# Kernel optimization log

Measured on AMD Instinct MI355X. Metric: run time of the kernel, lower is better.

Reference implementation:

```python
import jax, jax.numpy as jnp
import numpy as np

HIDDEN = 3072
HEADS = 24
HEAD_DIM = HIDDEN // HEADS  # 128
MLP_HIDDEN = 4 * HIDDEN     # 12288
IMG_LEN = 1024
TXT_LEN = 256
L = IMG_LEN + TXT_LEN
B = 1
EPS = 1e-6


def setup_inputs() -> dict:
    key = jax.random.key(0)
    ks = jax.random.split(key, 12)
    x = jax.random.normal(ks[0], (B, L, HIDDEN), jnp.float32)
    vec = jax.random.normal(ks[1], (B, HIDDEN), jnp.float32)
    # RoPE tables: real cos/sin of position * inv_freq, repeated over pairs (full head_dim)
    inv_freq = 1.0 / (10000.0 ** (np.arange(0, HEAD_DIM, 2, dtype=np.float32) / HEAD_DIM))
    theta = np.arange(IMG_LEN, dtype=np.float32)[:, None] * inv_freq[None, :]  # [img_len, D/2]
    theta = np.repeat(theta, 2, axis=-1)  # [img_len, D]
    freqs_cos = jnp.asarray(np.cos(theta))[None, :, None, :]  # [1, img_len, 1, D]
    freqs_sin = jnp.asarray(np.sin(theta))[None, :, None, :]
    s = 0.02
    mod_w = jax.random.normal(ks[2], (HIDDEN, 3 * HIDDEN), jnp.float32) * s
    mod_b = jnp.zeros((3 * HIDDEN,), jnp.float32)
    w1 = jax.random.normal(ks[3], (HIDDEN, 3 * HIDDEN + MLP_HIDDEN), jnp.float32) * s
    b1 = jnp.zeros((3 * HIDDEN + MLP_HIDDEN,), jnp.float32)
    w2 = jax.random.normal(ks[4], (HIDDEN + MLP_HIDDEN, HIDDEN), jnp.float32) * s
    b2 = jnp.zeros((HIDDEN,), jnp.float32)
    qn_w = jnp.ones((HEAD_DIM,), jnp.float32)
    kn_w = jnp.ones((HEAD_DIM,), jnp.float32)
    cu_seqlens_q = jnp.array([0, IMG_LEN, L], jnp.int32)
    cu_seqlens_kv = jnp.array([0, IMG_LEN, L], jnp.int32)
    return {"x": x, "vec": vec, "freqs_cos": freqs_cos, "freqs_sin": freqs_sin,
            "mod_w": mod_w, "mod_b": mod_b, "w1": w1, "b1": b1, "w2": w2, "b2": b2,
            "qn_w": qn_w, "kn_w": kn_w, "img_len": IMG_LEN,
            "cu_seqlens_q": cu_seqlens_q, "cu_seqlens_kv": cu_seqlens_kv}


def _layernorm(x):  # elementwise_affine=False
    mu = jnp.mean(x, axis=-1, keepdims=True)
    var = jnp.mean(jnp.square(x - mu), axis=-1, keepdims=True)
    return (x - mu) * jax.lax.rsqrt(var + EPS)


def _rmsnorm(x, w):
    ms = jnp.mean(jnp.square(x), axis=-1, keepdims=True)
    return x * jax.lax.rsqrt(ms + EPS) * w


def _rope_interleaved(x, cos, sin):
    # mode=1: rotate interleaved pairs: (-x1, x0, -x3, x2, ...)
    x0 = x[..., 0::2]
    x1 = x[..., 1::2]
    rot = jnp.stack([-x1, x0], axis=-1).reshape(x.shape)
    return x * cos + rot * sin


def reference(x, vec, freqs_cos, freqs_sin, mod_w, mod_b, w1, b1, w2, b2,
              qn_w, kn_w, img_len, cu_seqlens_q, cu_seqlens_kv):
    bs = x.shape[0]
    assert cu_seqlens_q.shape[0] == 2 * bs + 1
    # adaLN modulation: SiLU -> Linear(hidden, 3*hidden)
    mod = jax.nn.silu(vec) @ mod_w + mod_b           # [B, 3H]
    mod = mod[:, None, :]                             # [B, 1, 3H]
    mod_shift, mod_scale, mod_gate = jnp.split(mod, 3, axis=-1)
    x_mod = _layernorm(x) * (1.0 + mod_scale) + mod_shift
    # fused QKV + MLP projection
    h = x_mod @ w1 + b1                               # [B, L, 3*hidden + mlp]
    qkv = h[..., :3 * HIDDEN]
    mlp = h[..., 3 * HIDDEN:]
    # 'B L (K H D) -> K B L H D'
    qkv = qkv.reshape(bs, -1, 3, HEADS, HEAD_DIM)
    q, k, v = qkv[:, :, 0], qkv[:, :, 1], qkv[:, :, 2]  # [B, L, H, D]
    q = _rmsnorm(q, qn_w)
    k = _rmsnorm(k, kn_w)
    # RoPE on image tokens only
    img_q = _rope_interleaved(q[:, :img_len], freqs_cos, freqs_sin)
    img_k = _rope_interleaved(k[:, :img_len], freqs_cos, freqs_sin)
    q = jnp.concatenate([img_q, q[:, img_len:]], axis=1)
    k = jnp.concatenate([img_k, k[:, img_len:]], axis=1)
    # dense attention (bs==1 path, no mask), scale = 1/sqrt(head_dim)
    scale = 1.0 / jnp.sqrt(jnp.float32(HEAD_DIM))
    scores = jnp.einsum('bqhd,bkhd->bhqk', q, k) * scale
    probs = jax.nn.softmax(scores, axis=-1)
    attn = jnp.einsum('bhqk,bkhd->bqhd', probs, v)
    attn = attn.reshape(bs, -1, HEADS * HEAD_DIM)     # [B, L, hidden]
    # output projection on concat(attn, gelu_tanh(mlp))
    out = jnp.concatenate([attn, jax.nn.gelu(mlp, approximate=True)], axis=-1) @ w2 + b2
    return x + out * mod_gate
```

## Files before the change

### kernel.cpp

```cpp
#include <hip/hip_runtime.h>
#include <cstdint>
#include <cstddef>

typedef __bf16 bf16x8_t __attribute__((ext_vector_type(8)));
typedef float f32x4 __attribute__((ext_vector_type(4)));

#define HID 3072
#define NHEADS 24
#define HD 128
#define MLP 12288
#define SEQ 1280
#define IMG 1024
#define N1 21504
#define QKVW 9216
#define A2W 15360
#define EPSV 1e-6f

__device__ __forceinline__ size_t tpos(int row, int col, int KT) {
    return ((size_t)(row >> 8) * KT + (col >> 6)) * 16384
         + (size_t)(((((col >> 5) & 1) << 4) + ((row >> 4) & 15)) * 512
                    + (((row & 15) + (((col >> 3) & 3) << 4)) << 3) + (col & 7));
}

__device__ __forceinline__ void gload16(const void* g, void* l) {
    __builtin_amdgcn_global_load_lds(
        (const __attribute__((address_space(1))) unsigned int*)g,
        (__attribute__((address_space(3))) unsigned int*)l, 16, 0, 0);
}

__device__ __forceinline__ void bar() {
    asm volatile("" ::: "memory");
    __builtin_amdgcn_s_barrier();
    asm volatile("" ::: "memory");
}

__device__ __forceinline__ float bf2f(uint u) {
    return __builtin_bit_cast(float, u << 16);
}
__device__ __forceinline__ ushort f2bfu(float f) {
    return __builtin_bit_cast(ushort, (__bf16)f);
}

__device__ __forceinline__ void conv_tile(const float* __restrict__ in, ushort* __restrict__ out,
                                          int N, int KT, int kb, int nb, int tid,
                                          float (*tle)[65]) {
    int k0 = kb * 64, n0 = nb * 64;
    int rr = tid >> 2, cg = (tid & 3) * 16;
    #pragma unroll
    for (int j = 0; j < 4; ++j) {
        float4 vv = *reinterpret_cast<const float4*>(&in[(size_t)(k0 + rr) * N + n0 + cg + j * 4]);
        tle[rr][cg + j * 4 + 0] = vv.x;
        tle[rr][cg + j * 4 + 1] = vv.y;
        tle[rr][cg + j * 4 + 2] = vv.z;
        tle[rr][cg + j * 4 + 3] = vv.w;
    }
    __syncthreads();
    int nl = tid & 63;
    #pragma unroll
    for (int gg = 0; gg < 2; ++gg) {
        int g = (tid >> 6) + gg * 4;
        union { ushort u[8]; uint4 q; } pk;
        #pragma unroll
        for (int j = 0; j < 8; ++j)
            pk.u[j] = f2bfu(tle[g * 8 + j][nl]);
        *reinterpret_cast<uint4*>(&out[tpos(n0 + nl, k0 + g * 8, KT)]) = pk.q;
    }
}

__global__ void silu_kernel(const float* __restrict__ v, float* __restrict__ sv) {
    int i = blockIdx.x * 256 + threadIdx.x;
    float x = v[i];
    sv[i] = x / (1.f + expf(-x));
}

__global__ __launch_bounds__(256) void gemvconv_fat(const float* __restrict__ sv,
                                                    const float* __restrict__ W,
                                                    float* __restrict__ part,
                                                    const float* __restrict__ w1,
                                                    ushort* __restrict__ w1b) {
    __shared__ float tle[64][65];
    int bid = blockIdx.x;
    int tid = threadIdx.x;
    if (bid < 288) {
        int n = (bid % 36) * 256 + tid;
        int k0 = (bid / 36) * 384;
        float s = 0.f;
        for (int k = k0; k < k0 + 384; ++k)
            s = fmaf(sv[k], W[(size_t)k * QKVW + n], s);
        part[(size_t)(bid / 36) * QKVW + n] = s;
        return;
    }
    int cb = bid - 288;
    conv_tile(w1, w1b, N1, HID / 64, cb % 48, cb / 48, tid, tle);
}

__global__ void gemv_reduce(const float* __restrict__ part, const float* __restrict__ bias,
                            float* __restrict__ mod) {
    int n = blockIdx.x * 256 + threadIdx.x;
    float s = bias[n];
    #pragma unroll
    for (int ky = 0; ky < 8; ++ky) s += part[(size_t)ky * QKVW + n];
    mod[n] = s;
}

__global__ __launch_bounds__(384) void ln_mod_kernel(const float* __restrict__ x,
                                                     const float* __restrict__ mod,
                                                     ushort* __restrict__ xmt) {
    int m = blockIdx.x;
    int t = threadIdx.x;
    int lane = t & 63, w = t >> 6;
    const float* xr = x + (size_t)m * HID;
    float4 v0 = *reinterpret_cast<const float4*>(&xr[t * 8]);
    float4 v1 = *reinterpret_cast<const float4*>(&xr[t * 8 + 4]);
    float s = v0.x + v0.y + v0.z + v0.w + v1.x + v1.y + v1.z + v1.w;
    float sq = v0.x * v0.x + v0.y * v0.y + v0.z * v0.z + v0.w * v0.w +
               v1.x * v1.x + v1.y * v1.y + v1.z * v1.z + v1.w * v1.w;
    #pragma unroll
    for (int off = 1; off < 64; off <<= 1) {
        s += __shfl_xor(s, off);
        sq += __shfl_xor(sq, off);
    }
    __shared__ float red[12];
    if (lane == 0) { red[w] = s; red[w + 6] = sq; }
    __syncthreads();
    s = red[0] + red[1] + red[2] + red[3] + red[4] + red[5];
    sq = red[6] + red[7] + red[8] + red[9] + red[10] + red[11];
    float mu = s * (1.f / HID);
    float var = sq * (1.f / HID) - mu * mu;
    float rs = rsqrtf(var + EPSV);
    float vals[8] = {v0.x, v0.y, v0.z, v0.w, v1.x, v1.y, v1.z, v1.w};
    union { ushort u[8]; uint4 q; } pk;
    #pragma unroll
    for (int j = 0; j < 8; ++j) {
        int n = t * 8 + j;
        float y = (vals[j] - mu) * rs * (1.f + mod[HID + n]) + mod[n];
        pk.u[j] = f2bfu(y);
    }
    *reinterpret_cast<uint4*>(&xmt[tpos(m, t * 8, HID >> 6)]) = pk.q;
}

template <int EPI, int SPLITS>
__global__ __launch_bounds__(512, 2) void gemmk(
    const ushort* __restrict__ At, const ushort* __restrict__ Bt,
    const float* __restrict__ bias, ushort* __restrict__ out1, ushort* __restrict__ out2,
    int KT64, int NT32, int NTN) {
    int nwg = gridDim.x;
    int q = nwg >> 3, r = nwg & 7;
    int orig = blockIdx.x;
    int xcd = orig & 7;
    int wgid = (xcd < r ? xcd * (q + 1) : r * (q + 1) + (xcd - r) * q) + (orig >> 3);
    int mt = wgid % 5;
    int p = wgid / 5;
    int nt = p % NTN;
    int sp = p / NTN;
    int kOff = sp * NT32;
    int m0 = mt * 256, n0 = nt * 256;

    __shared__ ushort LA[4][8192];
    __shared__ ushort LB[4][8192];

    int tid = threadIdx.x;
    int lane = tid & 63, wid = tid >> 6;
    int wm = wid >> 2, wn = wid & 3;
    int lr = lane & 15, lg = lane >> 4;

    const ushort* gA = At + (size_t)mt * KT64 * 16384;
    const ushort* gB = Bt + (size_t)nt * KT64 * 16384;

    f32x4 acc[8][4] = {};
    bf16x8_t af[8], bf[4];

    auto stage = [&](int sl, int tt) {
        size_t base = (size_t)(tt >> 1) * 16384 + (size_t)(tt & 1) * 8192;
        #pragma unroll
        for (int j = 0; j < 2; ++j) {
            int b = wid * 2 + j;
            gload16(gA + base + b * 512 + lane * 8, &LA[sl][b * 512]);
            gload16(gB + base + b * 512 + lane * 8, &LB[sl][b * 512]);
        }
    };

    stage(0, kOff); stage(1, kOff + 1); stage(2, kOff + 2); stage(3, kOff + 3);
    asm volatile("s_waitcnt vmcnt(12)" ::: "memory");
    bar();

    for (int t = 0; t < NT32; ++t) {
        int sl = t & 3;
        #pragma unroll
        for (int mi = 0; mi < 8; ++mi)
            af[mi] = *reinterpret_cast<const bf16x8_t*>(&LA[sl][(wm * 8 + mi) * 512 + lane * 8]);
        #pragma unroll
        for (int nj = 0; nj < 4; ++nj)
            bf[nj] = *reinterpret_cast<const bf16x8_t*>(&LB[sl][(wn * 4 + nj) * 512 + lane * 8]);
        __builtin_amdgcn_s_setprio(1);
        #pragma unroll
        for (int mi = 0; mi < 8; ++mi)
            #pragma unroll
            for (int nj = 0; nj < 4; ++nj)
                acc[mi][nj] = __builtin_amdgcn_mfma_f32_16x16x32_bf16(af[mi], bf[nj], acc[mi][nj], 0, 0, 0);
        __builtin_amdgcn_s_setprio(0);
        bar();
        if (t + 4 < NT32) {
            stage(sl, kOff + t + 4);
            asm volatile("s_waitcnt vmcnt(12)" ::: "memory");
        } else if (t + 3 < NT32) {
            asm volatile("s_waitcnt vmcnt(8)" ::: "memory");
        } else if (t + 2 < NT32) {
            asm volatile("s_waitcnt vmcnt(4)" ::: "memory");
        } else if (t + 1 < NT32) {
            asm volatile("s_waitcnt vmcnt(0)" ::: "memory");
        }
        bar();
    }

    #pragma unroll
    for (int mi = 0; mi < 8; ++mi) {
        #pragma unroll
        for (int nj = 0; nj < 4; ++nj) {
            int col = n0 + wn * 64 + nj * 16 + lr;
            #pragma unroll
            for (int rr2 = 0; rr2 < 4; ++rr2) {
                int row = m0 + wm * 128 + mi * 16 + lg * 4 + rr2;
                float val = acc[mi][nj][rr2];
                if (EPI == 1) {
                    val += bias[col];
                    if (n0 < QKVW) {
                        out1[(size_t)row * QKVW + col] = f2bfu(val);
                    } else {
                        float u = 0.7978845608028654f * (val + 0.044715f * val * val * val);
                        float g = val / (1.f + __expf(-2.f * u));
                        out2[tpos(row, HID + (col - QKVW), A2W >> 6)] = f2bfu(g);
                    }
                } else {
                    out1[(size_t)(sp * SEQ + row) * HID + col] = f2bfu(val);
                }
            }
        }
    }
}

__global__ __launch_bounds__(256) void ksplit_reduce(const ushort* __restrict__ partb,
                                                     const float* __restrict__ x,
                                                     const float* __restrict__ bias,
                                                     const float* __restrict__ gate,
                                                     float* __restrict__ out) {
    size_t i = (size_t)blockIdx.x * 256 + threadIdx.x;
    int col = (int)((i * 8) % HID);
    float a[8] = {};
    #pragma unroll
    for (int s = 0; s < 4; ++s) {
        uint4 pv = *reinterpret_cast<const uint4*>(&partb[(size_t)s * SEQ * HID + i * 8]);
        uint w[4] = {pv.x, pv.y, pv.z, pv.w};
        #pragma unroll
        for (int c = 0; c < 4; ++c) {
            a[c * 2]     += bf2f(w[c] & 0xffffu);
            a[c * 2 + 1] += __builtin_bit_cast(float, w[c] & 0xffff0000u);
        }
    }
    f32x4 o0, o1;
    #pragma unroll
    for (int j = 0; j < 4; ++j) {
        o0[j] = x[i * 8 + j] + (a[j] + bias[col + j]) * gate[col + j];
        o1[j] = x[i * 8 + 4 + j] + (a[4 + j] + bias[col + 4 + j]) * gate[col + 4 + j];
    }
    *reinterpret_cast<f32x4*>(&out[i * 8]) = o0;
    *reinterpret_cast<f32x4*>(&out[i * 8 + 4]) = o1;
}

__global__ __launch_bounds__(256) void qkv_post(const ushort* __restrict__ hb,
                                                const float* __restrict__ fc,
                                                const float* __restrict__ fs,
                                                const float* __restrict__ qn,
                                                const float* __restrict__ kn,
                                                __bf16* __restrict__ qb,
                                                __bf16* __restrict__ kb,
                                                __bf16* __restrict__ vb) {
    int m = blockIdx.x;
    int lane = threadIdx.x & 63, w = threadIdx.x >> 6;
    for (int rr = w; rr < 72; rr += 4) {
        int s = rr / 24, hd = rr % 24;
        const ushort* src = hb + (size_t)m * QKVW + s * HID + hd * HD;
        uint pair = *reinterpret_cast<const uint*>(&src[2 * lane]);
        float x0 = bf2f(pair & 0xffffu);
        float x1 = __builtin_bit_cast(float, pair & 0xffff0000u);
        if (s < 2) {
            float ss = x0 * x0 + x1 * x1;
            #pragma unroll
            for (int off = 1; off < 64; off <<= 1) ss += __shfl_xor(ss, off);
            float rs = rsqrtf(ss * (1.f / HD) + EPSV);
            const float* nw = (s == 0) ? qn : kn;
            x0 *= rs * nw[2 * lane];
            x1 *= rs * nw[2 * lane + 1];
            if (m < IMG) {
                float c0 = fc[m * HD + 2 * lane], c1 = fc[m * HD + 2 * lane + 1];
                float s0 = fs[m * HD + 2 * lane], s1 = fs[m * HD + 2 * lane + 1];
                float r0 = x0 * c0 - x1 * s0;
                float r1 = x1 * c1 + x0 * s1;
                x0 = r0; x1 = r1;
            }
        }
        __bf16* dst = ((s == 0) ? qb : (s == 1) ? kb : vb) + (size_t)hd * SEQ * HD + (size_t)m * HD + 2 * lane;
        uint u0 = f2bfu(x0), u1 = f2bfu(x1);
        *reinterpret_cast<uint*>(dst) = u0 | (u1 << 16);
    }
}

__global__ __launch_bounds__(256) void attn_fat(const __bf16* __restrict__ qb,
                                                const __bf16* __restrict__ kb,
                                                const __bf16* __restrict__ vb,
                                                ushort* __restrict__ a2,
                                                const float* __restrict__ w2,
                                                ushort* __restrict__ w2b) {
    __shared__ float tle[64][65];
    int bid = blockIdx.x;
    int tid = threadIdx.x;
    if (bid >= 480) {
        int cb = bid - 480;
        conv_tile(w2, w2b, HID, A2W / 64, cb % 240, cb / 240, tid, tle);
        return;
    }
    __shared__ alignas(16) __bf16 Kl[32][136];
    __shared__ alignas(16) __bf16 Vl[32][136];
    __shared__ float Pl[4][32][16];

    int head = bid / 20;
    int lane = tid & 63, w = tid >> 6;
    int lr = lane & 15, lg = lane >> 4;
    int q0 = (bid % 20) * 64 + w * 16;
    const __bf16* Q = qb + (size_t)head * SEQ * HD;
    const __bf16* Kp = kb + (size_t)head * SEQ * HD;
    const __bf16* Vp = vb + (size_t)head * SEQ * HD;

    bf16x8_t qf[4];
    #pragma unroll
    for (int kc = 0; kc < 4; ++kc)
        qf[kc] = *reinterpret_cast<const bf16x8_t*>(&Q[(size_t)(q0 + lr) * HD + kc * 32 + lg * 8]);

    float m_run = -1e30f, l_run = 0.f;
    f32x4 of[8] = {};
    const float sm_scale = 0.08838834764831845f;

    for (int kv0 = 0; kv0 < SEQ; kv0 += 32) {
        #pragma unroll
        for (int cc = 0; cc < 2; ++cc) {
            int c = tid + cc * 256;
            int row = c >> 4, off = (c & 15) * 8;
            *reinterpret_cast<bf16x8_t*>(&Kl[row][off]) =
                *reinterpret_cast<const bf16x8_t*>(&Kp[(size_t)(kv0 + row) * HD + off]);
            *reinterpret_cast<bf16x8_t*>(&Vl[row][off]) =
                *reinterpret_cast<const bf16x8_t*>(&Vp[(size_t)(kv0 + row) * HD + off]);
        }
        __syncthreads();

        f32x4 st[2] = {};
        #pragma unroll
        for (int h = 0; h < 2; ++h)
            #pragma unroll
            for (int kc = 0; kc < 4; ++kc) {
                bf16x8_t kf = *reinterpret_cast<const bf16x8_t*>(&Kl[h * 16 + lr][kc * 32 + lg * 8]);
                st[h] = __builtin_amdgcn_mfma_f32_16x16x32_bf16(kf, qf[kc], st[h], 0, 0, 0);
            }
        float sarr[8];
        #pragma unroll
        for (int h = 0; h < 2; ++h)
            #pragma unroll
            for (int r = 0; r < 4; ++r) sarr[h * 4 + r] = st[h][r] * sm_scale;

        float mloc = sarr[0];
        #pragma unroll
        for (int i = 1; i < 8; ++i) mloc = fmaxf(mloc, sarr[i]);
        mloc = fmaxf(mloc, __shfl_xor(mloc, 16));
        mloc = fmaxf(mloc, __shfl_xor(mloc, 32));
        float m_new = fmaxf(m_run, mloc);
        float alpha = expf(m_run - m_new);
        float pv[8], psum = 0.f;
        #pragma unroll
        for (int i = 0; i < 8; ++i) { pv[i] = expf(sarr[i] - m_new); psum += pv[i]; }
        psum += __shfl_xor(psum, 16);
        psum += __shfl_xor(psum, 32);
        l_run = l_run * alpha + psum;
        m_run = m_new;

        #pragma unroll
        for (int h = 0; h < 2; ++h)
            #pragma unroll
            for (int r = 0; r < 4; ++r) Pl[w][h * 16 + lg * 4 + r][lr] = pv[h * 4 + r];
        bf16x8_t pa;
        #pragma unroll
        for (int j = 0; j < 8; ++j) pa[j] = (__bf16)Pl[w][lg * 8 + j][lr];

        float alr[4];
        #pragma unroll
        for (int r = 0; r < 4; ++r) alr[r] = __shfl(alpha, lg * 4 + r);

        #pragma unroll
        for (int db = 0; db < 8; ++db) {
            #pragma unroll
            for (int r = 0; r < 4; ++r) of[db][r] *= alr[r];
            bf16x8_t vv;
            #pragma unroll
            for (int j = 0; j < 8; ++j) vv[j] = Vl[lg * 8 + j][db * 16 + lr];
            of[db] = __builtin_amdgcn_mfma_f32_16x16x32_bf16(pa, vv, of[db], 0, 0, 0);
        }
        __syncthreads();
    }

    float lr4[4];
    #pragma unroll
    for (int r = 0; r < 4; ++r) lr4[r] = __shfl(l_run, lg * 4 + r);
    #pragma unroll
    for (int db = 0; db < 8; ++db)
        #pragma unroll
        for (int r = 0; r < 4; ++r) {
            int row = q0 + lg * 4 + r;
            int col = head * HD + db * 16 + lr;
            a2[tpos(row, col, A2W >> 6)] = f2bfu(of[db][r] / lr4[r]);
        }
}

extern "C" void kernel_launch(void* const* d_in, const int* in_sizes, int n_in,
                              void* d_out, int out_size, void* d_ws, size_t ws_size,
                              hipStream_t stream) {
    const float* x = (const float*)d_in[0];
    const float* vec = (const float*)d_in[1];
    const float* fc = (const float*)d_in[2];
    const float* fs = (const float*)d_in[3];
    const float* mod_w = (const float*)d_in[4];
    const float* mod_b = (const float*)d_in[5];
    const float* w1 = (const float*)d_in[6];
    const float* b1 = (const float*)d_in[7];
    const float* w2 = (const float*)d_in[8];
    const float* b2 = (const float*)d_in[9];
    const float* qn = (const float*)d_in[10];
    const float* kn = (const float*)d_in[11];
    float* out = (float*)d_out;

    char* ws = (char*)d_ws;
    size_t off = 0;
    float* sv = (float*)(ws + off); off += 3072 * 4;
    float* mod = (float*)(ws + off); off += 9216 * 4;
    float* part = (float*)(ws + off); off += 8 * 9216 * 4;
    off = (off + 255) & ~(size_t)255;
    ushort* xmt = (ushort*)(ws + off); off += (size_t)SEQ * HID * 2;
    off = (off + 255) & ~(size_t)255;
    ushort* hqkvb = (ushort*)(ws + off); off += (size_t)SEQ * QKVW * 2;
    __bf16* qb = (__bf16*)(ws + off); off += (size_t)NHEADS * SEQ * HD * 2;
    __bf16* kb = (__bf16*)(ws + off); off += (size_t)NHEADS * SEQ * HD * 2;
    __bf16* vb = (__bf16*)(ws + off); off += (size_t)NHEADS * SEQ * HD * 2;
    off = (off + 255) & ~(size_t)255;
    ushort* a2t = (ushort*)(ws + off); off += (size_t)SEQ * A2W * 2;
    ushort* partb = hqkvb;

    off = (off + 255) & ~(size_t)255;
    ushort* w1b = (ushort*)(ws + off);
    ushort* w2b = w1b;

    silu_kernel<<<12, 256, 0, stream>>>(vec, sv);
    gemvconv_fat<<<288 + 48 * 336, 256, 0, stream>>>(sv, mod_w, part, w1, w1b);
    gemv_reduce<<<36, 256, 0, stream>>>(part, mod_b, mod);
    ln_mod_kernel<<<SEQ, 384, 0, stream>>>(x, mod, xmt);

    gemmk<1, 1><<<5 * (N1 / 256), 512, 0, stream>>>(xmt, w1b, b1, hqkvb, a2t,
                                                    HID / 64, HID / 32, N1 / 256);
    qkv_post<<<SEQ, 256, 0, stream>>>(hqkvb, fc, fs, qn, kn, qb, kb, vb);
    attn_fat<<<480 + 240 * 48, 256, 0, stream>>>(qb, kb, vb, a2t, w2, w2b);
    gemmk<2, 4><<<4 * 5 * (HID / 256), 512, 0, stream>>>(a2t, w2b, nullptr, partb, nullptr,
                                                         A2W / 64, A2W / 32 / 4, HID / 256);
    ksplit_reduce<<<SEQ * HID / 2048, 256, 0, stream>>>(partb, x, b2, mod + 2 * HID, out);
}
```

Before: 731.9 us.

## Replace 256x256 GEMM with 128x128 tile kernel using quadrant-split ping-pong schedule

After: 702.3 us. 4.0% less time.

```diff
diff --git a/kernel.cpp b/kernel.cpp
--- a/kernel.cpp
+++ b/kernel.cpp
@@ -140,88 +140,116 @@
 }
 
 template <int EPI, int SPLITS>
-__global__ __launch_bounds__(512, 2) void gemmk(
+__global__ __launch_bounds__(256, 2) void gemm128(
     const ushort* __restrict__ At, const ushort* __restrict__ Bt,
     const float* __restrict__ bias, ushort* __restrict__ out1, ushort* __restrict__ out2,
-    int KT64, int NT32, int NTN) {
+    int KT64, int NTloc, int NTN, int MB) {
     int nwg = gridDim.x;
     int q = nwg >> 3, r = nwg & 7;
     int orig = blockIdx.x;
     int xcd = orig & 7;
     int wgid = (xcd < r ? xcd * (q + 1) : r * (q + 1) + (xcd - r) * q) + (orig >> 3);
-    int mt = wgid % 5;
-    int p = wgid / 5;
+    int mt = wgid % MB;
+    int p = wgid / MB;
     int nt = p % NTN;
     int sp = p / NTN;
-    int kOff = sp * NT32;
-    int m0 = mt * 256, n0 = nt * 256;
-
-    __shared__ ushort LA[4][8192];
-    __shared__ ushort LB[4][8192];
+    int kOff = sp * NTloc;
+    int m0 = mt * 128, n0 = nt * 128;
+    int hA = (mt & 1) * 8, hB = (nt & 1) * 8;
+
+    __shared__ ushort LA[2][8192];
+    __shared__ ushort LB[2][8192];
 
     int tid = threadIdx.x;
     int lane = tid & 63, wid = tid >> 6;
-    int wm = wid >> 2, wn = wid & 3;
+    int wm = wid >> 1, wn = wid & 1;
     int lr = lane & 15, lg = lane >> 4;
 
-    const ushort* gA = At + (size_t)mt * KT64 * 16384;
-    const ushort* gB = Bt + (size_t)nt * KT64 * 16384;
-
-    f32x4 acc[8][4] = {};
-    bf16x8_t af[8], bf[4];
-
-    auto stage = [&](int sl, int tt) {
-        size_t base = (size_t)(tt >> 1) * 16384 + (size_t)(tt & 1) * 8192;
-        #pragma unroll
-        for (int j = 0; j < 2; ++j) {
-            int b = wid * 2 + j;
-            gload16(gA + base + b * 512 + lane * 8, &LA[sl][b * 512]);
-            gload16(gB + base + b * 512 + lane * 8, &LB[sl][b * 512]);
+    const ushort* gA = At + (size_t)(mt >> 1) * KT64 * 16384;
+    const ushort* gB = Bt + (size_t)(nt >> 1) * KT64 * 16384;
+
+    f32x4 acc[4][4] = {};
+    bf16x8_t af0[2][2], af1[2][2], bf0[2][2], bf1[2][2];
+
+    auto stage = [&](ushort (*L)[8192], int buf, const ushort* g, int kt, int h0) {
+        #pragma unroll
+        for (int j = 0; j < 4; ++j) {
+            int lb = wid * 4 + j;
+            int b = ((lb >> 3) << 4) + h0 + (lb & 7);
+            gload16(g + (size_t)kt * 16384 + b * 512 + lane * 8, &L[buf][lb * 512]);
         }
     };
-
-    stage(0, kOff); stage(1, kOff + 1); stage(2, kOff + 2); stage(3, kOff + 3);
-    asm volatile("s_waitcnt vmcnt(12)" ::: "memory");
+    auto rdA = [&](int buf, int h, bf16x8_t (&af)[2][2]) {
+        #pragma unroll
+        for (int mi = 0; mi < 2; ++mi)
+            #pragma unroll
+            for (int k = 0; k < 2; ++k)
+                af[mi][k] = *reinterpret_cast<const bf16x8_t*>(
+                    &LA[buf][(k * 8 + wm * 4 + h * 2 + mi) * 512 + lane * 8]);
+    };
+    auto rdB = [&](int buf, int v, bf16x8_t (&bf)[2][2]) {
+        #pragma unroll
+        for (int ni = 0; ni < 2; ++ni)
+            #pragma unroll
+            for (int k = 0; k < 2; ++k)
+                bf[ni][k] = *reinterpret_cast<const bf16x8_t*>(
+                    &LB[buf][(k * 8 + wn * 4 + v * 2 + ni) * 512 + lane * 8]);
+    };
+    auto mmq = [&](bf16x8_t (&af)[2][2], bf16x8_t (&bf)[2][2], int h, int v) {
+        __builtin_amdgcn_s_setprio(1);
+        #pragma unroll
+        for (int mi = 0; mi < 2; ++mi)
+            #pragma unroll
+            for (int ni = 0; ni < 2; ++ni)
+                #pragma unroll
+                for (int k = 0; k < 2; ++k)
+                    acc[h * 2 + mi][v * 2 + ni] = __builtin_amdgcn_mfma_f32_16x16x32_bf16(
+                        af[mi][k], bf[ni][k], acc[h * 2 + mi][v * 2 + ni], 0, 0, 0);
+        __builtin_amdgcn_s_setprio(0);
+    };
+
+    stage(LA, 0, gA, kOff, hA);
+    stage(LB, 0, gB, kOff, hB);
+    stage(LA, 1, gA, kOff + 1, hA);
+    stage(LB, 1, gB, kOff + 1, hB);
+    asm volatile("s_waitcnt vmcnt(8)" ::: "memory");
     bar();
-
-    for (int t = 0; t < NT32; ++t) {
-        int sl = t & 3;
-        #pragma unroll
-        for (int mi = 0; mi < 8; ++mi)
-            af[mi] = *reinterpret_cast<const bf16x8_t*>(&LA[sl][(wm * 8 + mi) * 512 + lane * 8]);
-        #pragma unroll
-        for (int nj = 0; nj < 4; ++nj)
-            bf[nj] = *reinterpret_cast<const bf16x8_t*>(&LB[sl][(wn * 4 + nj) * 512 + lane * 8]);
-        __builtin_amdgcn_s_setprio(1);
-        #pragma unroll
-        for (int mi = 0; mi < 8; ++mi)
-            #pragma unroll
-            for (int nj = 0; nj < 4; ++nj)
-                acc[mi][nj] = __builtin_amdgcn_mfma_f32_16x16x32_bf16(af[mi], bf[nj], acc[mi][nj], 0, 0, 0);
-        __builtin_amdgcn_s_setprio(0);
+    rdA(0, 0, af0);
+    rdB(0, 0, bf0);
+
+    for (int t = 0; t < NTloc; ++t) {
+        int c = t & 1;
+        rdB(c, 1, bf1);
+        mmq(af0, bf0, 0, 0);
         bar();
-        if (t + 4 < NT32) {
-            stage(sl, kOff + t + 4);
-            asm volatile("s_waitcnt vmcnt(12)" ::: "memory");
-        } else if (t + 3 < NT32) {
-            asm volatile("s_waitcnt vmcnt(8)" ::: "memory");
-        } else if (t + 2 < NT32) {
-            asm volatile("s_waitcnt vmcnt(4)" ::: "memory");
-        } else if (t + 1 < NT32) {
-            asm volatile("s_waitcnt vmcnt(0)" ::: "memory");
-        }
+        rdA(c, 1, af1);
+        mmq(af0, bf1, 0, 1);
         bar();
-    }
-
-    #pragma unroll
-    for (int mi = 0; mi < 8; ++mi) {
+        if (t + 2 < NTloc) stage(LA, c, gA, kOff + t + 2, hA);
+        mmq(af1, bf0, 1, 0);
+        if (t + 1 < NTloc) {
+            if (t + 2 < NTloc) asm volatile("s_waitcnt vmcnt(4)" ::: "memory");
+            else               asm volatile("s_waitcnt vmcnt(0)" ::: "memory");
+        }
+        bar();
+        if (t + 1 < NTloc) {
+            rdA(c ^ 1, 0, af0);
+            rdB(c ^ 1, 0, bf0);
+        }
+        if (t + 2 < NTloc) stage(LB, c, gB, kOff + t + 2, hB);
+        mmq(af1, bf1, 1, 1);
+        bar();
+    }
+
+    #pragma unroll
+    for (int fi = 0; fi < 4; ++fi) {
         #pragma unroll
         for (int nj = 0; nj < 4; ++nj) {
             int col = n0 + wn * 64 + nj * 16 + lr;
             #pragma unroll
             for (int rr2 = 0; rr2 < 4; ++rr2) {
-                int row = m0 + wm * 128 + mi * 16 + lg * 4 + rr2;
-                float val = acc[mi][nj][rr2];
+                int row = m0 + wm * 64 + fi * 16 + lg * 4 + rr2;
+                float val = acc[fi][nj][rr2];
                 if (EPI == 1) {
                     val += bias[col];
                     if (n0 < QKVW) {
@@ -460,11 +488,11 @@
     gemv_reduce<<<36, 256, 0, stream>>>(part, mod_b, mod);
     ln_mod_kernel<<<SEQ, 384, 0, stream>>>(x, mod, xmt);
 
-    gemmk<1, 1><<<5 * (N1 / 256), 512, 0, stream>>>(xmt, w1b, b1, hqkvb, a2t,
-                                                    HID / 64, HID / 32, N1 / 256);
+    gemm128<1, 1><<<10 * (N1 / 128), 256, 0, stream>>>(xmt, w1b, b1, hqkvb, a2t,
+                                                       HID / 64, HID / 64, N1 / 128, 10);
     qkv_post<<<SEQ, 256, 0, stream>>>(hqkvb, fc, fs, qn, kn, qb, kb, vb);
     attn_fat<<<480 + 240 * 48, 256, 0, stream>>>(qb, kb, vb, a2t, w2, w2b);
-    gemmk<2, 4><<<4 * 5 * (HID / 256), 512, 0, stream>>>(a2t, w2b, nullptr, partb, nullptr,
-                                                         A2W / 64, A2W / 32 / 4, HID / 256);
+    gemm128<2, 4><<<4 * 10 * (HID / 128), 256, 0, stream>>>(a2t, w2b, nullptr, partb, nullptr,
+                                                            A2W / 64, A2W / 64 / 4, HID / 128, 10);
     ksplit_reduce<<<SEQ * HID / 2048, 256, 0, stream>>>(partb, x, b2, mod + 2 * HID, out);
 }
```
